# Kernel tuning notes

Hardware: AMD Instinct MI355X
Metric: run time of the kernel (lower is better)

## Reference

```python
import jax, jax.numpy as jnp
import numpy as np


def _gcn_conv(x, edge_index, W, b):
    """PyG-style GCNConv: linear, add self-loops, symmetric norm, scatter-add, bias."""
    n = x.shape[0]
    h = x @ W  # [N, F_out]
    loops = jnp.arange(n, dtype=edge_index.dtype)
    row = jnp.concatenate([edge_index[0], loops])  # source
    col = jnp.concatenate([edge_index[1], loops])  # target
    deg = jax.ops.segment_sum(jnp.ones_like(col, dtype=h.dtype), col, num_segments=n)
    dinv = jnp.where(deg > 0, jax.lax.rsqrt(deg), 0.0)
    norm = dinv[row] * dinv[col]  # [E+N]
    msg = h[row] * norm[:, None]  # edge-wise gather + scale
    out = jax.ops.segment_sum(msg, col, num_segments=n)  # scatter-add
    return out + b


def setup_inputs() -> dict:
    key = jax.random.key(0)
    k1, k2, k3, k4 = jax.random.split(key, 4)
    N, E, F_in, F_out = 50000, 800000, 128, 64
    hidden = 2 * F_out
    x = jax.random.normal(k1, (N, F_in), dtype=jnp.float32)
    edge_index = jax.random.randint(k2, (2, E), 0, N, dtype=jnp.int64)
    # Glorot-ish init for weights
    W1 = jax.random.normal(k3, (F_in, hidden), dtype=jnp.float32) / np.sqrt(F_in)
    b1 = jnp.zeros((hidden,), dtype=jnp.float32)
    W2 = jax.random.normal(k4, (hidden, F_out), dtype=jnp.float32) / np.sqrt(hidden)
    b2 = jnp.zeros((F_out,), dtype=jnp.float32)
    return {"x": x, "edge_index": edge_index, "W1": W1, "b1": b1, "W2": W2, "b2": b2}


def reference(x, edge_index, W1, b1, W2, b2):
    h = _gcn_conv(x, edge_index, W1, b1)
    h = jax.nn.relu(h)
    out = _gcn_conv(h, edge_index, W2, b2)
    return out
```

## Files before the change

### kernel.cpp

```cpp
#include <hip/hip_runtime.h>
#include <stdint.h>


typedef _Float16 h2v   __attribute__((ext_vector_type(2)));
typedef _Float16 h4v   __attribute__((ext_vector_type(4)));
typedef _Float16 f16x8 __attribute__((ext_vector_type(8)));
typedef float    f32x4 __attribute__((ext_vector_type(4)));

#if defined(__has_builtin)
#if __has_builtin(__builtin_amdgcn_fdot2)
#define HAVE_FDOT2 1
#endif
#endif

__device__ __forceinline__ float fdot2_acc(h2v a, h2v b, float c) {
#ifdef HAVE_FDOT2
    return __builtin_amdgcn_fdot2(a, b, c, false);
#else
    return c + (float)a.x * (float)b.x + (float)a.y * (float)b.y;
#endif
}
__device__ __forceinline__ h2v as_h2(uint32_t u) { return __builtin_bit_cast(h2v, u); }

__global__ void k_prep(const float* __restrict__ W1, const float* __restrict__ W2,
                       _Float16* __restrict__ WT1, h2v* __restrict__ W2P,
                       uint32_t* __restrict__ bcnt,
                       _Float16* __restrict__ h1, _Float16* __restrict__ h2, int n) {
    int i = blockIdx.x * blockDim.x + threadIdx.x;
    if (i < 256) bcnt[i] = 0u;
    if (i < 128) h1[(size_t)n * 128 + i] = (_Float16)0.f;
    if (i < 64)  h2[(size_t)n * 64  + i] = (_Float16)0.f;
    if (i < 128 * 128) {
        int f = i >> 7, k = i & 127;
        WT1[i] = (_Float16)W1[k * 128 + f];
    }
    if (i < 4096) {
        int k2 = i >> 6, f = i & 63;
        h2v pr;
        pr.x = (_Float16)W2[(2 * k2) * 64 + f];
        pr.y = (_Float16)W2[(2 * k2 + 1) * 64 + f];
        W2P[i] = pr;
    }
}

__global__ __launch_bounds__(256)
void k_bhist(const int* __restrict__ col, uint32_t* __restrict__ bcnt, int E) {
    __shared__ uint32_t h[256];
    const int t = threadIdx.x;
    h[t] = 0u; __syncthreads();
    const int base = blockIdx.x * 4096;
#pragma unroll
    for (int k = 0; k < 16; ++k) {
        int i = base + k * 256 + t;
        if (i < E) atomicAdd(&h[__builtin_nontemporal_load(&col[i]) >> 8], 1u);
    }
    __syncthreads();
    if (h[t]) atomicAdd(&bcnt[t], h[t]);
}

__global__ void k_bscan(const uint32_t* __restrict__ bcnt, uint32_t* __restrict__ boff,
                        uint32_t* __restrict__ bfill, int NB) {
    __shared__ uint32_t s[256];
    const int t = threadIdx.x;
    uint32_t v = (t < NB) ? bcnt[t] : 0u;
    s[t] = v; __syncthreads();
    for (int off = 1; off < 256; off <<= 1) {
        uint32_t u = (t >= off) ? s[t - off] : 0u;
        __syncthreads();
        s[t] += u;
        __syncthreads();
    }
    uint32_t ex = s[t] - v;
    if (t < NB) { boff[t] = ex; bfill[t] = ex; }
    if (t == NB - 1) boff[NB] = s[t];
}

__global__ __launch_bounds__(256)
void k_bin(const int* __restrict__ row, const int* __restrict__ col,
           uint32_t* __restrict__ bfill, uint32_t* __restrict__ ebuf, int E) {
    __shared__ uint32_t hcnt[256], hbase[256];
    const int t = threadIdx.x;
    hcnt[t] = 0u; __syncthreads();
    const int base = blockIdx.x * 4096;
#pragma unroll
    for (int k = 0; k < 16; ++k) {
        int i = base + k * 256 + t;
        if (i < E) atomicAdd(&hcnt[__builtin_nontemporal_load(&col[i]) >> 8], 1u);
    }
    __syncthreads();
    hbase[t] = atomicAdd(&bfill[t], hcnt[t]);
    hcnt[t] = 0u;
    __syncthreads();
#pragma unroll
    for (int k = 0; k < 16; ++k) {
        int i = base + k * 256 + t;
        if (i < E) {
            int c = __builtin_nontemporal_load(&col[i]);
            int r = __builtin_nontemporal_load(&row[i]);
            int b = c >> 8;
            uint32_t slot = hbase[b] + atomicAdd(&hcnt[b], 1u);
            ebuf[slot] = (uint32_t)r | ((uint32_t)(c & 255) << 16);
        }
    }
}

__global__ __launch_bounds__(256)
void k_bucket(const uint32_t* __restrict__ boff, const uint32_t* __restrict__ ebuf,
              uint32_t* __restrict__ rps, uint32_t* __restrict__ rpe,
              float* __restrict__ dinv, uint16_t* __restrict__ esrc, int n) {
    __shared__ uint32_t lcnt[256], lscan[256], lbase[256], lfill[256];
    __shared__ uint32_t s_total;
    const int t = threadIdx.x;
    const int b = blockIdx.x;
    const int base_c = b << 8;
    const int nc = min(256, n - base_c);
    const uint32_t start = boff[b], end = boff[b + 1];
    const uint32_t pstart = (start + (uint32_t)b * 2048u + 7u) & ~7u;

    lcnt[t] = 0u; __syncthreads();
    for (uint32_t i = start + t; i < end; i += 256)
        atomicAdd(&lcnt[ebuf[i] >> 16], 1u);
    __syncthreads();

    const uint32_t v  = lcnt[t];
    const uint32_t pc = (v + 7u) & ~7u;
    lscan[t] = pc; __syncthreads();
    for (int off = 1; off < 256; off <<= 1) {
        uint32_t u = (t >= off) ? lscan[t - off] : 0u;
        __syncthreads();
        lscan[t] += u;
        __syncthreads();
    }
    const uint32_t pex = lscan[t] - pc;
    if (t == 255) s_total = lscan[255];
    if (t < nc) {
        rps[base_c + t]  = pstart + pex;
        rpe[base_c + t]  = pstart + pex + pc;
        dinv[base_c + t] = rsqrtf((float)(v + 1u));
    }
    lbase[t] = pstart + pex;
    lfill[t] = 0u;
    __syncthreads();
    const uint32_t total = s_total;
    for (uint32_t i = t; i < total; i += 256)
        esrc[pstart + i] = (uint16_t)n;
    __syncthreads();
    for (uint32_t i = start + t; i < end; i += 256) {
        uint32_t vv = ebuf[i];
        uint32_t cl = vv >> 16;
        uint32_t slot = lbase[cl] + atomicAdd(&lfill[cl], 1u);
        esrc[slot] = (uint16_t)(vv & 0xffffu);
    }
}

template <int FOUT, typename XT>
__global__ __launch_bounds__(256)
void k_gemm_mfma(const XT* __restrict__ X, const _Float16* __restrict__ WT,
                 const float* __restrict__ dinv, _Float16* __restrict__ H, int n) {
    constexpr int K  = 128;
    constexpr int KP = K + 8;
    constexpr int NT = FOUT / 16;
    __shared__ _Float16 Wl[FOUT * KP];

    const int tid = threadIdx.x;
    for (int i = tid; i < FOUT * (K / 8); i += 256) {
        int f = i / (K / 8), kc = i % (K / 8);
        *reinterpret_cast<f16x8*>(&Wl[f * KP + kc * 8]) =
            *reinterpret_cast<const f16x8*>(&WT[f * K + kc * 8]);
    }
    __syncthreads();

    const int wid  = tid >> 6;
    const int lane = tid & 63;
    const int col  = lane & 15;
    const int krow = lane >> 4;
    const int node = blockIdx.x * 64 + wid * 16 + col;
    const int nld  = node < n ? node : n - 1;

    f32x4 acc[NT];
#pragma unroll
    for (int t = 0; t < NT; ++t) acc[t] = (f32x4){0.f, 0.f, 0.f, 0.f};

#pragma unroll
    for (int ks = 0; ks < 4; ++ks) {
        const int k0 = ks * 32 + krow * 8;
        f16x8 b;
        if constexpr (sizeof(XT) == 4) {
            float4 x0 = *reinterpret_cast<const float4*>(&X[(size_t)nld * K + k0]);
            float4 x1 = *reinterpret_cast<const float4*>(&X[(size_t)nld * K + k0 + 4]);
            b[0] = (_Float16)x0.x; b[1] = (_Float16)x0.y;
            b[2] = (_Float16)x0.z; b[3] = (_Float16)x0.w;
            b[4] = (_Float16)x1.x; b[5] = (_Float16)x1.y;
            b[6] = (_Float16)x1.z; b[7] = (_Float16)x1.w;
        } else {
            b = *reinterpret_cast<const f16x8*>(&X[(size_t)nld * K + k0]);
        }
#pragma unroll
        for (int t = 0; t < NT; ++t) {
            f16x8 a = *reinterpret_cast<const f16x8*>(&Wl[(t * 16 + col) * KP + k0]);
            acc[t] = __builtin_amdgcn_mfma_f32_16x16x32_f16(a, b, acc[t], 0, 0, 0);
        }
    }

    if (node < n) {
        const float dv = dinv[node];
#pragma unroll
        for (int t = 0; t < NT; ++t) {
            h4v hv;
            hv.x = (_Float16)(acc[t][0] * dv);
            hv.y = (_Float16)(acc[t][1] * dv);
            hv.z = (_Float16)(acc[t][2] * dv);
            hv.w = (_Float16)(acc[t][3] * dv);
            *reinterpret_cast<h4v*>(&H[(size_t)node * FOUT + t * 16 + krow * 4]) = hv;
        }
    }
}

__global__ __launch_bounds__(256)
void k_aggmm(const _Float16* __restrict__ H, const uint32_t* __restrict__ rps,
             const uint32_t* __restrict__ rpe, const uint16_t* __restrict__ es,
             const float* __restrict__ dinv, const float* __restrict__ b1,
             const h2v* __restrict__ W2P, _Float16* __restrict__ h2out, int n) {
    __shared__ h2v      W2l[64 * 64];
    __shared__ _Float16 g1row[4][128];
    const int tid = threadIdx.x;
    for (int i = tid; i < 1024; i += 256)
        reinterpret_cast<uint4*>(W2l)[i] = reinterpret_cast<const uint4*>(W2P)[i];
    __syncthreads();

    const int wid = tid >> 6, lane = tid & 63;
    const int v = blockIdx.x * 4 + wid;
    if (v >= n) return;
    const uint32_t shift = (lane & 32) ? 16u : 0u;
    const uint32_t loff  = (uint32_t)(lane & 31) * 8u;
    const char* Hb = (const char*)H;
    const h2v one0 = {(_Float16)1.f, (_Float16)0.f};
    const h2v zero1 = {(_Float16)0.f, (_Float16)1.f};

    int p = (int)rps[v];
    const int e = (int)rpe[v];
    float a0 = 0.f, a1 = 0.f, a2 = 0.f, a3 = 0.f;

    for (; p + 8 <= e; p += 8) {
        const uint4 wa = *reinterpret_cast<const uint4*>(&es[p]);
        uint32_t dw[4] = {wa.x, wa.y, wa.z, wa.w};
#pragma unroll
        for (int j = 0; j < 4; ++j) {
            uint32_t id  = (dw[j] >> shift) & 0xffffu;
            uint32_t off = (id << 8) + loff;
            uint2 u = *reinterpret_cast<const uint2*>(Hb + off);
            h2v lo = as_h2(u.x), hi = as_h2(u.y);
            a0 = fdot2_acc(lo, one0,  a0);
            a1 = fdot2_acc(lo, zero1, a1);
            a2 = fdot2_acc(hi, one0,  a2);
            a3 = fdot2_acc(hi, zero1, a3);
        }
    }
    a0 += __shfl_xor(a0, 32); a1 += __shfl_xor(a1, 32);
    a2 += __shfl_xor(a2, 32); a3 += __shfl_xor(a3, 32);

    {
        uint2 su = *reinterpret_cast<const uint2*>(Hb + ((uint32_t)v << 8) + loff);
        h2v lo = as_h2(su.x), hi = as_h2(su.y);
        a0 = fdot2_acc(lo, one0,  a0);
        a1 = fdot2_acc(lo, zero1, a1);
        a2 = fdot2_acc(hi, one0,  a2);
        a3 = fdot2_acc(hi, zero1, a3);
    }
    const float dv = dinv[v];
    const float4 bv = *reinterpret_cast<const float4*>(&b1[(lane & 31) * 4]);
    h4v gh;
    gh.x = (_Float16)fmaxf(fmaf(dv, a0, bv.x), 0.f);
    gh.y = (_Float16)fmaxf(fmaf(dv, a1, bv.y), 0.f);
    gh.z = (_Float16)fmaxf(fmaf(dv, a2, bv.z), 0.f);
    gh.w = (_Float16)fmaxf(fmaf(dv, a3, bv.w), 0.f);
    *reinterpret_cast<h4v*>(&g1row[wid][(lane & 31) * 4]) = gh;

    float acc = 0.f;
#pragma unroll
    for (int kb = 0; kb < 64; kb += 4) {
        uint4 gu = *reinterpret_cast<const uint4*>(&g1row[wid][kb * 2]);
        acc = fdot2_acc(W2l[(kb + 0) * 64 + lane], as_h2(gu.x), acc);
        acc = fdot2_acc(W2l[(kb + 1) * 64 + lane], as_h2(gu.y), acc);
        acc = fdot2_acc(W2l[(kb + 2) * 64 + lane], as_h2(gu.z), acc);
        acc = fdot2_acc(W2l[(kb + 3) * 64 + lane], as_h2(gu.w), acc);
    }
    h2out[(size_t)v * 64 + lane] = (_Float16)(dv * acc);
}

__global__ __launch_bounds__(256)
void k_agg64(const _Float16* __restrict__ H, const uint32_t* __restrict__ rps,
             const uint32_t* __restrict__ rpe, const uint16_t* __restrict__ es,
             const float* __restrict__ dinv, const float* __restrict__ bias,
             float* __restrict__ out, int n) {
    int wave = (blockIdx.x * blockDim.x + threadIdx.x) >> 6;
    int lane = threadIdx.x & 63;
    if (wave >= n) return;
    const int v = wave;
    const bool seldw   = (lane & 32) != 0;
    const uint32_t shift = (lane & 16) ? 16u : 0u;
    const uint32_t loff  = (uint32_t)(lane & 15) * 8u;
    const char* Hb = (const char*)H;
    const h2v one0 = {(_Float16)1.f, (_Float16)0.f};
    const h2v zero1 = {(_Float16)0.f, (_Float16)1.f};

    int p = (int)rps[v];
    const int e = (int)rpe[v];
    float a0 = 0.f, a1 = 0.f, a2 = 0.f, a3 = 0.f;

    for (; p + 8 <= e; p += 8) {
        const uint4 wa = *reinterpret_cast<const uint4*>(&es[p]);
        uint32_t d0 = seldw ? wa.y : wa.x;
        uint32_t d1 = seldw ? wa.w : wa.z;
#pragma unroll
        for (int j = 0; j < 2; ++j) {
            uint32_t d = j ? d1 : d0;
            uint32_t id  = (d >> shift) & 0xffffu;
            uint32_t off = (id << 7) + loff;
            uint2 u = *reinterpret_cast<const uint2*>(Hb + off);
            h2v lo = as_h2(u.x), hi = as_h2(u.y);
            a0 = fdot2_acc(lo, one0,  a0);
            a1 = fdot2_acc(lo, zero1, a1);
            a2 = fdot2_acc(hi, one0,  a2);
            a3 = fdot2_acc(hi, zero1, a3);
        }
    }
    a0 += __shfl_xor(a0, 16); a1 += __shfl_xor(a1, 16);
    a2 += __shfl_xor(a2, 16); a3 += __shfl_xor(a3, 16);
    a0 += __shfl_xor(a0, 32); a1 += __shfl_xor(a1, 32);
    a2 += __shfl_xor(a2, 32); a3 += __shfl_xor(a3, 32);

    if (lane < 16) {
        uint2 su = *reinterpret_cast<const uint2*>(Hb + ((uint32_t)v << 7) + loff);
        h2v lo = as_h2(su.x), hi = as_h2(su.y);
        a0 = fdot2_acc(lo, one0,  a0);
        a1 = fdot2_acc(lo, zero1, a1);
        a2 = fdot2_acc(hi, one0,  a2);
        a3 = fdot2_acc(hi, zero1, a3);
        const float dv = dinv[v];
        const float4 bv = *reinterpret_cast<const float4*>(&bias[lane * 4]);
        float4 o;
        o.x = fmaf(dv, a0, bv.x);
        o.y = fmaf(dv, a1, bv.y);
        o.z = fmaf(dv, a2, bv.z);
        o.w = fmaf(dv, a3, bv.w);
        *reinterpret_cast<float4*>(&out[(size_t)v * 64 + lane * 4]) = o;
    }
}

extern "C" void kernel_launch(void* const* d_in, const int* in_sizes, int n_in,
                              void* d_out, int out_size, void* d_ws, size_t ws_size,
                              hipStream_t stream) {
    const float* x  = (const float*)d_in[0];
    const int*   ei = (const int*)d_in[1];
    const float* W1 = (const float*)d_in[2];
    const float* b1 = (const float*)d_in[3];
    const float* W2 = (const float*)d_in[4];
    const float* b2 = (const float*)d_in[5];
    float* out = (float*)d_out;

    const int hidden = in_sizes[3];
    const int fin    = in_sizes[2] / hidden;
    const int n      = in_sizes[0] / fin;
    const int E      = in_sizes[1] / 2;
    const int* rowi = ei;
    const int* coli = ei + E;
    (void)n_in; (void)out_size; (void)ws_size;

    char* ws = (char*)d_ws;
    size_t off = 0;
    auto alloc = [&](size_t bytes) -> void* {
        off = (off + 255) & ~(size_t)255;
        void* p = ws + off;
        off += bytes;
        return p;
    };
    const int NB = (n + 255) >> 8;
    uint32_t*  bcnt = (uint32_t*) alloc(256 * 4);
    uint32_t*  boff = (uint32_t*) alloc(257 * 4);
    uint32_t*  bfill= (uint32_t*) alloc(256 * 4);
    uint32_t*  rps  = (uint32_t*) alloc((size_t)n * 4);
    uint32_t*  rpe  = (uint32_t*) alloc((size_t)n * 4);
    float*     dinv = (float*)    alloc((size_t)n * 4);
    uint32_t*  ebuf = (uint32_t*) alloc((size_t)E * 4);
    uint16_t*  esrc = (uint16_t*) alloc(((size_t)E + (size_t)NB * 2048 + 4096) * 2);
    _Float16*  h1   = (_Float16*) alloc((size_t)(n + 1) * 128 * 2);
    _Float16*  h2   = (_Float16*) alloc((size_t)(n + 1) * 64 * 2);
    _Float16*  WT1  = (_Float16*) alloc(128 * 128 * 2);
    h2v*       W2P  = (h2v*)      alloc(64 * 64 * sizeof(h2v));

    const int NW = (E + 4095) >> 12;

    k_prep  <<<64, 256, 0, stream>>>(W1, W2, WT1, W2P, bcnt, h1, h2, n);
    k_bhist <<<NW, 256, 0, stream>>>(coli, bcnt, E);
    k_bscan <<<1, 256, 0, stream>>>(bcnt, boff, bfill, NB);
    k_bin   <<<NW, 256, 0, stream>>>(rowi, coli, bfill, ebuf, E);
    k_bucket<<<NB, 256, 0, stream>>>(boff, ebuf, rps, rpe, dinv, esrc, n);

    const int gb = (n + 63) / 64;
    k_gemm_mfma<128, float><<<gb, 256, 0, stream>>>(x, WT1, dinv, h1, n);
    k_aggmm <<<(n + 3) / 4, 256, 0, stream>>>(h1, rps, rpe, esrc, dinv, b1, W2P, h2, n);
    k_agg64 <<<(n + 3) / 4, 256, 0, stream>>>(h2, rps, rpe, esrc, dinv, b2, out, n);
}
```

Baseline: 207.5 us.

## Pad edge lists to 16, batch gathers, process four nodes per wave in aggmm

Per-node edge segments are now padded to multiples of 16 instead of 8. Both aggregation kernels load 16 indices per iteration and issue all neighbor gathers before accumulating, so more memory loads are in flight at once. k_aggmm now handles four nodes per wave, which amortizes the shared-memory load of W2 over more nodes and launches a quarter as many blocks. The second matmul uses four independent accumulators. In exchange, the extra padding adds dummy gathers for low-degree nodes and enlarges the esrc buffer. There are also fewer waves available to hide latency.

New measurement: 194.2 us. 6.4% less time.

```diff
diff --git a/kernel.cpp b/kernel.cpp
--- a/kernel.cpp
+++ b/kernel.cpp
@@ -115,7 +115,7 @@
     const int base_c = b << 8;
     const int nc = min(256, n - base_c);
     const uint32_t start = boff[b], end = boff[b + 1];
-    const uint32_t pstart = (start + (uint32_t)b * 2048u + 7u) & ~7u;
+    const uint32_t pstart = (start + (uint32_t)b * 4096u + 15u) & ~15u;
 
     lcnt[t] = 0u; __syncthreads();
     for (uint32_t i = start + t; i < end; i += 256)
@@ -123,7 +123,7 @@
     __syncthreads();
 
     const uint32_t v  = lcnt[t];
-    const uint32_t pc = (v + 7u) & ~7u;
+    const uint32_t pc = (v + 15u) & ~15u;
     lscan[t] = pc; __syncthreads();
     for (int off = 1; off < 256; off <<= 1) {
         uint32_t u = (t >= off) ? lscan[t - off] : 0u;
@@ -229,63 +229,79 @@
     __syncthreads();
 
     const int wid = tid >> 6, lane = tid & 63;
-    const int v = blockIdx.x * 4 + wid;
-    if (v >= n) return;
+    const int v0 = blockIdx.x * 16 + wid * 4;
+    if (v0 >= n) return;
     const uint32_t shift = (lane & 32) ? 16u : 0u;
     const uint32_t loff  = (uint32_t)(lane & 31) * 8u;
     const char* Hb = (const char*)H;
-    const h2v one0 = {(_Float16)1.f, (_Float16)0.f};
+    const h2v one0  = {(_Float16)1.f, (_Float16)0.f};
     const h2v zero1 = {(_Float16)0.f, (_Float16)1.f};
-
-    int p = (int)rps[v];
-    const int e = (int)rpe[v];
-    float a0 = 0.f, a1 = 0.f, a2 = 0.f, a3 = 0.f;
-
-    for (; p + 8 <= e; p += 8) {
-        const uint4 wa = *reinterpret_cast<const uint4*>(&es[p]);
-        uint32_t dw[4] = {wa.x, wa.y, wa.z, wa.w};
-#pragma unroll
-        for (int j = 0; j < 4; ++j) {
-            uint32_t id  = (dw[j] >> shift) & 0xffffu;
-            uint32_t off = (id << 8) + loff;
-            uint2 u = *reinterpret_cast<const uint2*>(Hb + off);
-            h2v lo = as_h2(u.x), hi = as_h2(u.y);
+    const float4 bv = *reinterpret_cast<const float4*>(&b1[(lane & 31) * 4]);
+
+    const uint4  rs4 = *reinterpret_cast<const uint4*>(&rps[v0]);
+    const uint4  re4 = *reinterpret_cast<const uint4*>(&rpe[v0]);
+    const float4 dv4 = *reinterpret_cast<const float4*>(&dinv[v0]);
+    const uint32_t pss[4] = {rs4.x, rs4.y, rs4.z, rs4.w};
+    const uint32_t pes[4] = {re4.x, re4.y, re4.z, re4.w};
+    const float    dvs[4] = {dv4.x, dv4.y, dv4.z, dv4.w};
+
+#pragma unroll
+    for (int ni = 0; ni < 4; ++ni) {
+        const int v = v0 + ni;
+        if (v >= n) break;
+        uint32_t p = pss[ni];
+        const uint32_t e = pes[ni];
+        float a0 = 0.f, a1 = 0.f, a2 = 0.f, a3 = 0.f;
+
+        for (; p < e; p += 16) {
+            const uint4 wa = *reinterpret_cast<const uint4*>(&es[p]);
+            const uint4 wb = *reinterpret_cast<const uint4*>(&es[p + 8]);
+            uint32_t dw[8] = {wa.x, wa.y, wa.z, wa.w, wb.x, wb.y, wb.z, wb.w};
+            uint2 u[8];
+#pragma unroll
+            for (int j = 0; j < 8; ++j) {
+                uint32_t id = (dw[j] >> shift) & 0xffffu;
+                u[j] = *reinterpret_cast<const uint2*>(Hb + (id << 8) + loff);
+            }
+#pragma unroll
+            for (int j = 0; j < 8; ++j) {
+                h2v lo = as_h2(u[j].x), hi = as_h2(u[j].y);
+                a0 = fdot2_acc(lo, one0,  a0);
+                a1 = fdot2_acc(lo, zero1, a1);
+                a2 = fdot2_acc(hi, one0,  a2);
+                a3 = fdot2_acc(hi, zero1, a3);
+            }
+        }
+        a0 += __shfl_xor(a0, 32); a1 += __shfl_xor(a1, 32);
+        a2 += __shfl_xor(a2, 32); a3 += __shfl_xor(a3, 32);
+
+        {
+            uint2 su = *reinterpret_cast<const uint2*>(Hb + ((uint32_t)v << 8) + loff);
+            h2v lo = as_h2(su.x), hi = as_h2(su.y);
             a0 = fdot2_acc(lo, one0,  a0);
             a1 = fdot2_acc(lo, zero1, a1);
             a2 = fdot2_acc(hi, one0,  a2);
             a3 = fdot2_acc(hi, zero1, a3);
         }
-    }
-    a0 += __shfl_xor(a0, 32); a1 += __shfl_xor(a1, 32);
-    a2 += __shfl_xor(a2, 32); a3 += __shfl_xor(a3, 32);
-
-    {
-        uint2 su = *reinterpret_cast<const uint2*>(Hb + ((uint32_t)v << 8) + loff);
-        h2v lo = as_h2(su.x), hi = as_h2(su.y);
-        a0 = fdot2_acc(lo, one0,  a0);
-        a1 = fdot2_acc(lo, zero1, a1);
-        a2 = fdot2_acc(hi, one0,  a2);
-        a3 = fdot2_acc(hi, zero1, a3);
-    }
-    const float dv = dinv[v];
-    const float4 bv = *reinterpret_cast<const float4*>(&b1[(lane & 31) * 4]);
-    h4v gh;
-    gh.x = (_Float16)fmaxf(fmaf(dv, a0, bv.x), 0.f);
-    gh.y = (_Float16)fmaxf(fmaf(dv, a1, bv.y), 0.f);
-    gh.z = (_Float16)fmaxf(fmaf(dv, a2, bv.z), 0.f);
-    gh.w = (_Float16)fmaxf(fmaf(dv, a3, bv.w), 0.f);
-    *reinterpret_cast<h4v*>(&g1row[wid][(lane & 31) * 4]) = gh;
-
-    float acc = 0.f;
-#pragma unroll
-    for (int kb = 0; kb < 64; kb += 4) {
-        uint4 gu = *reinterpret_cast<const uint4*>(&g1row[wid][kb * 2]);
-        acc = fdot2_acc(W2l[(kb + 0) * 64 + lane], as_h2(gu.x), acc);
-        acc = fdot2_acc(W2l[(kb + 1) * 64 + lane], as_h2(gu.y), acc);
-        acc = fdot2_acc(W2l[(kb + 2) * 64 + lane], as_h2(gu.z), acc);
-        acc = fdot2_acc(W2l[(kb + 3) * 64 + lane], as_h2(gu.w), acc);
-    }
-    h2out[(size_t)v * 64 + lane] = (_Float16)(dv * acc);
+        const float dv = dvs[ni];
+        h4v gh;
+        gh.x = (_Float16)fmaxf(fmaf(dv, a0, bv.x), 0.f);
+        gh.y = (_Float16)fmaxf(fmaf(dv, a1, bv.y), 0.f);
+        gh.z = (_Float16)fmaxf(fmaf(dv, a2, bv.z), 0.f);
+        gh.w = (_Float16)fmaxf(fmaf(dv, a3, bv.w), 0.f);
+        *reinterpret_cast<h4v*>(&g1row[wid][(lane & 31) * 4]) = gh;
+
+        float c0 = 0.f, c1 = 0.f, c2 = 0.f, c3 = 0.f;
+#pragma unroll
+        for (int kb = 0; kb < 64; kb += 4) {
+            uint4 gu = *reinterpret_cast<const uint4*>(&g1row[wid][kb * 2]);
+            c0 = fdot2_acc(W2l[(kb + 0) * 64 + lane], as_h2(gu.x), c0);
+            c1 = fdot2_acc(W2l[(kb + 1) * 64 + lane], as_h2(gu.y), c1);
+            c2 = fdot2_acc(W2l[(kb + 2) * 64 + lane], as_h2(gu.z), c2);
+            c3 = fdot2_acc(W2l[(kb + 3) * 64 + lane], as_h2(gu.w), c3);
+        }
+        h2out[(size_t)v * 64 + lane] = (_Float16)(dv * ((c0 + c1) + (c2 + c3)));
+    }
 }
 
 __global__ __launch_bounds__(256)
@@ -297,28 +313,32 @@
     int lane = threadIdx.x & 63;
     if (wave >= n) return;
     const int v = wave;
-    const bool seldw   = (lane & 32) != 0;
-    const uint32_t shift = (lane & 16) ? 16u : 0u;
+    const int qi = (lane >> 4) & 3;
+    const bool sely = (qi >> 1) != 0;
+    const uint32_t shift = (qi & 1) ? 16u : 0u;
     const uint32_t loff  = (uint32_t)(lane & 15) * 8u;
     const char* Hb = (const char*)H;
-    const h2v one0 = {(_Float16)1.f, (_Float16)0.f};
+    const h2v one0  = {(_Float16)1.f, (_Float16)0.f};
     const h2v zero1 = {(_Float16)0.f, (_Float16)1.f};
 
-    int p = (int)rps[v];
-    const int e = (int)rpe[v];
+    uint32_t p = rps[v];
+    const uint32_t e = rpe[v];
     float a0 = 0.f, a1 = 0.f, a2 = 0.f, a3 = 0.f;
 
-    for (; p + 8 <= e; p += 8) {
+    for (; p < e; p += 16) {
         const uint4 wa = *reinterpret_cast<const uint4*>(&es[p]);
-        uint32_t d0 = seldw ? wa.y : wa.x;
-        uint32_t d1 = seldw ? wa.w : wa.z;
-#pragma unroll
-        for (int j = 0; j < 2; ++j) {
-            uint32_t d = j ? d1 : d0;
-            uint32_t id  = (d >> shift) & 0xffffu;
-            uint32_t off = (id << 7) + loff;
-            uint2 u = *reinterpret_cast<const uint2*>(Hb + off);
-            h2v lo = as_h2(u.x), hi = as_h2(u.y);
+        const uint4 wb = *reinterpret_cast<const uint4*>(&es[p + 8]);
+        uint32_t d[4] = { sely ? wa.y : wa.x, sely ? wa.w : wa.z,
+                          sely ? wb.y : wb.x, sely ? wb.w : wb.z };
+        uint2 u[4];
+#pragma unroll
+        for (int j = 0; j < 4; ++j) {
+            uint32_t id = (d[j] >> shift) & 0xffffu;
+            u[j] = *reinterpret_cast<const uint2*>(Hb + (id << 7) + loff);
+        }
+#pragma unroll
+        for (int j = 0; j < 4; ++j) {
+            h2v lo = as_h2(u[j].x), hi = as_h2(u[j].y);
             a0 = fdot2_acc(lo, one0,  a0);
             a1 = fdot2_acc(lo, zero1, a1);
             a2 = fdot2_acc(hi, one0,  a2);
@@ -383,7 +403,7 @@
     uint32_t*  rpe  = (uint32_t*) alloc((size_t)n * 4);
     float*     dinv = (float*)    alloc((size_t)n * 4);
     uint32_t*  ebuf = (uint32_t*) alloc((size_t)E * 4);
-    uint16_t*  esrc = (uint16_t*) alloc(((size_t)E + (size_t)NB * 2048 + 4096) * 2);
+    uint16_t*  esrc = (uint16_t*) alloc(((size_t)E + (size_t)NB * 4096 + 4096) * 2);
     _Float16*  h1   = (_Float16*) alloc((size_t)(n + 1) * 128 * 2);
     _Float16*  h2   = (_Float16*) alloc((size_t)(n + 1) * 64 * 2);
     _Float16*  WT1  = (_Float16*) alloc(128 * 128 * 2);
@@ -399,6 +419,6 @@
 
     const int gb = (n + 63) / 64;
     k_gemm_mfma<128, float><<<gb, 256, 0, stream>>>(x, WT1, dinv, h1, n);
-    k_aggmm <<<(n + 3) / 4, 256, 0, stream>>>(h1, rps, rpe, esrc, dinv, b1, W2P, h2, n);
+    k_aggmm <<<(n + 15) / 16, 256, 0, stream>>>(h1, rps, rpe, esrc, dinv, b1, W2P, h2, n);
     k_agg64 <<<(n + 3) / 4, 256, 0, stream>>>(h2, rps, rpe, esrc, dinv, b2, out, n);
 }
```
